# Kernel tuning notes

Measured on AMD Instinct MI355X. Metric: run time of the kernel, lower is better.

The kernel has to match this reference:

```python
import jax, jax.numpy as jnp
import numpy as np

K = 3
N_SENSOR = 10   # num_sensor N (forced by reshape(-1,10,10))
ADJ_N = 5       # adjacency size (forced by reshape(-1,5,5))
T_LEN = 4096    # seq_len
BATCH = 1024    # batch_size == num_of_filters (forced by output accumulation)


def _scaled_laplacian(W):
    # L_tilde = 2L/lambda_max - I, L = D - W (W symmetric -> eigvalsh valid)
    D = jnp.diag(jnp.sum(W, axis=1))
    L = D - W
    lam_max = jnp.max(jnp.linalg.eigvalsh(L))
    return (2.0 * L) / lam_max - jnp.eye(W.shape[0], dtype=W.dtype)


def _cheb_polynomials(L_tilde, K):
    polys = [jnp.eye(L_tilde.shape[0], dtype=L_tilde.dtype), L_tilde]
    for _ in range(2, K):
        polys.append(2.0 * (L_tilde @ polys[-1]) - polys[-2])
    return jnp.stack(polys[:K])  # (K, 5, 5)


def setup_inputs() -> dict:
    key = jax.random.key(0)
    kx, ka, ks, kt = jax.random.split(key, 4)
    x = jax.random.normal(kx, (T_LEN, BATCH, N_SENSOR), dtype=jnp.float32)
    W = jax.random.uniform(ka, (ADJ_N, ADJ_N), dtype=jnp.float32)
    # symmetric, zero-diagonal adjacency so the Laplacian is symmetric PSD-ish
    adj_mx = (W + W.T) * 0.5 * (1.0 - jnp.eye(ADJ_N, dtype=jnp.float32))
    spatial_attention = jax.random.uniform(ks, (BATCH, N_SENSOR, N_SENSOR), dtype=jnp.float32)
    Theta = jax.random.normal(kt, (K, N_SENSOR, BATCH), dtype=jnp.float32)  # (K, num_of_timesteps=10, num_of_filters=B)
    return {"x": x, "adj_mx": adj_mx, "spatial_attention": spatial_attention, "Theta": Theta}


def reference(x, adj_mx, spatial_attention, Theta):
    # adj path is detached in the torch code (cpu().detach().numpy())
    L_tilde = _scaled_laplacian(jax.lax.stop_gradient(adj_mx))
    cheb = _cheb_polynomials(L_tilde, K)                 # (K, 5, 5)
    T, B, N = x.shape                                    # (T, B, 10)
    x_t = jnp.swapaxes(x, 0, 2)                          # (10, B, T)
    sa = spatial_attention.reshape(-1, ADJ_N, ADJ_N)     # (4B, 5, 5)
    output = jnp.zeros((T, B, N), dtype=x.dtype)
    for k in range(K):
        T_k_with_at = (cheb[k] * sa).reshape(-1, N, N)   # (B, 10, 10)
        lhs = jnp.swapaxes(T_k_with_at, 0, 2)            # (10, 10, B)
        rhs = jnp.matmul(lhs, x_t)                       # (10, 10, B) @ (10, B, T) -> (10, 10, T)
        out_k = jnp.matmul(jnp.swapaxes(rhs, 1, 2), Theta[k])  # (10, T, 10) @ (10, B) -> (10, T, B)
        output = output + jnp.transpose(out_k, (1, 2, 0))       # (T, B, 10)
    return jax.nn.relu(output[..., None])                # (T, B, 10, 1)
```

## Files before the change

kernel.cpp:

```cpp
#include <hip/hip_runtime.h>
#include <math.h>

#define TLEN 4096
#define NB   1024
#define NS   10

typedef __attribute__((ext_vector_type(8))) short  s16x8;
typedef __attribute__((ext_vector_type(4))) float  f32x4;

__device__ void k0_body(const float* __restrict__ adj, float* __restrict__ ck) {
  float Wm[5][5], L[5][5];
  for (int r = 0; r < 5; ++r)
    for (int c = 0; c < 5; ++c) Wm[r][c] = adj[r*5+c];
  for (int r = 0; r < 5; ++r) {
    float d = 0.f;
    for (int c = 0; c < 5; ++c) d += Wm[r][c];
    for (int c = 0; c < 5; ++c) L[r][c] = (r==c ? d : 0.f) - Wm[r][c];
  }
  float v[5] = {0.7f, -1.1f, 0.9f, -0.8f, 1.3f};
  for (int it = 0; it < 96; ++it) {
    float w[5];
    for (int r = 0; r < 5; ++r) {
      float s = 0.f;
      for (int c = 0; c < 5; ++c) s += L[r][c]*v[c];
      w[r] = s;
    }
    float s = fabsf(w[0])+fabsf(w[1])+fabsf(w[2])+fabsf(w[3])+fabsf(w[4]);
    float inv = 1.f/s;
    for (int r = 0; r < 5; ++r) v[r] = w[r]*inv;
  }
  float num = 0.f, den = 0.f;
  for (int r = 0; r < 5; ++r) {
    float s = 0.f;
    for (int c = 0; c < 5; ++c) s += L[r][c]*v[c];
    num += v[r]*s; den += v[r]*v[r];
  }
  const float lam = num/den;
  float Lt[5][5];
  for (int r = 0; r < 5; ++r)
    for (int c = 0; c < 5; ++c)
      Lt[r][c] = 2.f*L[r][c]/lam - (r==c ? 1.f : 0.f);
  float T2[5][5];
  for (int r = 0; r < 5; ++r)
    for (int c = 0; c < 5; ++c) {
      float s = 0.f;
      for (int j = 0; j < 5; ++j) s += Lt[r][j]*Lt[j][c];
      T2[r][c] = 2.f*s - (r==c ? 1.f : 0.f);
    }
  for (int p = 0; p < 10; ++p)
    for (int n = 0; n < 10; ++n) {
      int m = (10*p+n) % 25, r = m/5, c = m%5;
      ck[0*100 + p*10+n] = (r==c ? 1.f : 0.f);
      ck[1*100 + p*10+n] = Lt[r][c];
      ck[2*100 + p*10+n] = T2[r][c];
    }
}

static __device__ __forceinline__ unsigned cvtpk(float lo, float hi) {
  unsigned r;
  asm("v_cvt_pk_bf16_f32 %0, %1, %2" : "=v"(r) : "v"(lo), "v"(hi));
  return r;
}
static __device__ __forceinline__ int swz(int P, int L) {
  return P*64 + (L ^ ((P ^ (P >> 2)) & 7));
}

#define KC 64
#define BUF_U32 10240

__global__ __launch_bounds__(384, 3) void ka_mfma(
    const float* __restrict__ x, const float* __restrict__ sa,
    const float* __restrict__ adj, float* __restrict__ ps,
    float* __restrict__ ck) {
  __shared__ __align__(16) unsigned lds[2*BUF_U32];
  const int tid = threadIdx.x;
  if (tid >= 320) {
    if (tid == 320 && blockIdx.x == 0 && blockIdx.y == 0) k0_body(adj, ck);
    return;
  }
  const int w  = tid >> 6;
  const int l  = tid & 63;
  const int t0 = blockIdx.x * 16;
  const int b0 = blockIdx.y * 512;
  const int n0 = 2*w, n1 = 2*w + 1;

  const int bp = tid / 10;
  const int rm = tid - bp*10;
  const int q  = rm >> 1;
  const int th = rm & 1;
  const int gq = rm;
  const int ksx = bp >> 4;
  const int kgx = (bp & 15) >> 2;
  const int jwx = bp & 3;

  f32x4 acc0 = {0.f,0.f,0.f,0.f}, acc1 = {0.f,0.f,0.f,0.f};
  float2 xlo[8], xhi[8], slo[5], shi[5];

  unsigned* cur = lds;
  unsigned* nxt = lds + BUF_U32;

  {
    const float* xb = x + (size_t)(t0 + th*8)*(NB*NS) + (size_t)(b0 + 2*bp)*NS + 2*q;
    #pragma unroll
    for (int r = 0; r < 8; ++r) {
      xlo[r] = *(const float2*)(xb + r*(NB*NS));
      xhi[r] = *(const float2*)(xb + r*(NB*NS) + NS);
    }
    const float* sb = sa + (size_t)(b0 + 2*bp)*100 + gq*10;
    #pragma unroll
    for (int e = 0; e < 5; ++e) {
      slo[e] = *(const float2*)(sb + 2*e);
      shi[e] = *(const float2*)(sb + 100 + 2*e);
    }
  }
  #pragma unroll
  for (int r = 0; r < 8; ++r) {
    const int L = kgx*16 + th*8 + r;
    cur[swz((2*q  )*2 + ksx, L)*4 + jwx] = cvtpk(xlo[r].x, xhi[r].x);
    cur[swz((2*q+1)*2 + ksx, L)*4 + jwx] = cvtpk(xlo[r].y, xhi[r].y);
  }
  #pragma unroll
  for (int e = 0; e < 5; ++e) {
    const int L = kgx*16 + gq;
    cur[5120 + swz((2*e  )*2 + ksx, L)*4 + jwx] = cvtpk(slo[e].x, shi[e].x);
    cur[5120 + swz((2*e+1)*2 + ksx, L)*4 + jwx] = cvtpk(slo[e].y, shi[e].y);
  }

  for (int c = 0; c < 8; ++c) {
    __syncthreads();
    if (c < 7) {
      const int bc = b0 + (c+1)*KC;
      const float* xb = x + (size_t)(t0 + th*8)*(NB*NS) + (size_t)(bc + 2*bp)*NS + 2*q;
      #pragma unroll
      for (int r = 0; r < 8; ++r) {
        xlo[r] = *(const float2*)(xb + r*(NB*NS));
        xhi[r] = *(const float2*)(xb + r*(NB*NS) + NS);
      }
      const float* sb = sa + (size_t)(bc + 2*bp)*100 + gq*10;
      #pragma unroll
      for (int e = 0; e < 5; ++e) {
        slo[e] = *(const float2*)(sb + 2*e);
        shi[e] = *(const float2*)(sb + 100 + 2*e);
      }
    }
    {
      const s16x8* XBf = (const s16x8*)cur;
      const s16x8* ASf = (const s16x8*)(cur + 5120);
      #pragma unroll
      for (int ks = 0; ks < 2; ++ks) {
        acc0 = __builtin_amdgcn_mfma_f32_16x16x32_bf16(
                 ASf[swz(n0*2+ks, l)], XBf[swz(n0*2+ks, l)], acc0, 0, 0, 0);
        acc1 = __builtin_amdgcn_mfma_f32_16x16x32_bf16(
                 ASf[swz(n1*2+ks, l)], XBf[swz(n1*2+ks, l)], acc1, 0, 0, 0);
      }
    }
    if (c < 7) {
      #pragma unroll
      for (int r = 0; r < 8; ++r) {
        const int L = kgx*16 + th*8 + r;
        nxt[swz((2*q  )*2 + ksx, L)*4 + jwx] = cvtpk(xlo[r].x, xhi[r].x);
        nxt[swz((2*q+1)*2 + ksx, L)*4 + jwx] = cvtpk(xlo[r].y, xhi[r].y);
      }
      #pragma unroll
      for (int e = 0; e < 5; ++e) {
        const int L = kgx*16 + gq;
        nxt[5120 + swz((2*e  )*2 + ksx, L)*4 + jwx] = cvtpk(slo[e].x, shi[e].x);
        nxt[5120 + swz((2*e+1)*2 + ksx, L)*4 + jwx] = cvtpk(slo[e].y, shi[e].y);
      }
      unsigned* t = cur; cur = nxt; nxt = t;
    }
  }
  const int pg = (l >> 4) * 4;
  float* pd = ps + ((size_t)blockIdx.y*TLEN + t0 + (l & 15))*100;
  #pragma unroll
  for (int r = 0; r < 4; ++r) {
    const int p = pg + r;
    if (p < 10) {
      pd[n0*10 + p] = acc0[r];
      pd[n1*10 + p] = acc1[r];
    }
  }
}

#define TT 8
__global__ __launch_bounds__(256) void kc_out(const float* __restrict__ theta,
    const float* __restrict__ ck, const float* __restrict__ ps,
    float* __restrict__ out) {
  __shared__ __align__(16) float S[TT*120];
  __shared__ float C[300];
  __shared__ __align__(16) float stg[2][2560];
  const int tid = threadIdx.x;
  const int t0 = blockIdx.x * TT;
  const int b  = blockIdx.y * 256 + tid;
  for (int j = tid; j < 300; j += 256) C[j] = ck[j];
  for (int j = tid; j < TT*100; j += 256) {
    const int tt = j / 100, q = j - tt*100;
    float s = 0.f;
    #pragma unroll
    for (int sl = 0; sl < 2; ++sl)
      s += ps[((size_t)sl*TLEN + (t0+tt))*100 + q];
    S[tt*120 + (q/10)*12 + (q - (q/10)*10)] = s;
  }
  __syncthreads();
  float W[10][10];
  #pragma unroll
  for (int p = 0; p < 10; ++p) {
    const float th0 = theta[          p*NB + b];
    const float th1 = theta[10*NB  +  p*NB + b];
    const float th2 = theta[20*NB  +  p*NB + b];
    #pragma unroll
    for (int nn = 0; nn < 10; ++nn)
      W[p][nn] = C[p*10+nn]*th0 + C[100+p*10+nn]*th1 + C[200+p*10+nn]*th2;
  }
  for (int tt = 0; tt < TT; ++tt) {
    float acc[10];
    #pragma unroll
    for (int nn = 0; nn < 10; ++nn) {
      const float4 s0 = *(const float4*)(S + tt*120 + nn*12);
      const float4 s1 = *(const float4*)(S + tt*120 + nn*12 + 4);
      const float2 s2 = *(const float2*)(S + tt*120 + nn*12 + 8);
      acc[nn] = s0.x*W[0][nn] + s0.y*W[1][nn] + s0.z*W[2][nn] + s0.w*W[3][nn]
              + s1.x*W[4][nn] + s1.y*W[5][nn] + s1.z*W[6][nn] + s1.w*W[7][nn]
              + s2.x*W[8][nn] + s2.y*W[9][nn];
    }
    float* sg = stg[tt & 1];
    #pragma unroll
    for (int nn = 0; nn < 10; ++nn)
      sg[tid*10 + nn] = fmaxf(acc[nn], 0.f);
    __syncthreads();
    const float4* sp = (const float4*)sg;
    float4* op = (float4*)(out + (size_t)(t0+tt)*(NB*NS)
                               + (size_t)blockIdx.y*2560);
    op[tid]       = sp[tid];
    op[tid + 256] = sp[tid + 256];
    if (tid < 128) op[tid + 512] = sp[tid + 512];
  }
}

extern "C" void kernel_launch(void* const* d_in, const int* in_sizes, int n_in,
                              void* d_out, int out_size, void* d_ws, size_t ws_size,
                              hipStream_t stream) {
  const float* x   = (const float*)d_in[0];
  const float* adj = (const float*)d_in[1];
  const float* sa  = (const float*)d_in[2];
  const float* th  = (const float*)d_in[3];
  float* out = (float*)d_out;
  float* ws  = (float*)d_ws;
  float* ck  = ws;
  float* ps  = ws + 1024;
  hipLaunchKernelGGL(ka_mfma, dim3(TLEN/16, 2), dim3(384), 0, stream,
                     x, sa, adj, ps, ck);
  hipLaunchKernelGGL(kc_out,  dim3(TLEN/TT, NB/256), dim3(256), 0, stream,
                     th, ck, ps, out);
}
```

Baseline: 98.50 us.

## Fuse MFMA contraction and output projection into one kernel per time tile

Merges the two kernels into one: each block now covers all 1024 batch rows for 16 timesteps, keeps the partial sums in shared memory instead of writing them to a global workspace, and computes the Theta/Chebyshev projection and ReLU output in the same block. The Laplacian power iteration is recomputed in every block by an otherwise idle thread, spread across the chunk loop so it runs alongside the MFMA work. The double-buffered LDS staging becomes a single buffer with an extra barrier per chunk. Nontemporal loads and stores are used for x and the output. The grid shrinks to 256 blocks, which may lower occupancy, and the extra syncs may expose load latency.

```diff
diff --git a/kernel.cpp b/kernel.cpp
--- a/kernel.cpp
+++ b/kernel.cpp
@@ -4,57 +4,13 @@
 #define TLEN 4096
 #define NB   1024
 #define NS   10
-
-typedef __attribute__((ext_vector_type(8))) short  s16x8;
-typedef __attribute__((ext_vector_type(4))) float  f32x4;
-
-__device__ void k0_body(const float* __restrict__ adj, float* __restrict__ ck) {
-  float Wm[5][5], L[5][5];
-  for (int r = 0; r < 5; ++r)
-    for (int c = 0; c < 5; ++c) Wm[r][c] = adj[r*5+c];
-  for (int r = 0; r < 5; ++r) {
-    float d = 0.f;
-    for (int c = 0; c < 5; ++c) d += Wm[r][c];
-    for (int c = 0; c < 5; ++c) L[r][c] = (r==c ? d : 0.f) - Wm[r][c];
-  }
-  float v[5] = {0.7f, -1.1f, 0.9f, -0.8f, 1.3f};
-  for (int it = 0; it < 96; ++it) {
-    float w[5];
-    for (int r = 0; r < 5; ++r) {
-      float s = 0.f;
-      for (int c = 0; c < 5; ++c) s += L[r][c]*v[c];
-      w[r] = s;
-    }
-    float s = fabsf(w[0])+fabsf(w[1])+fabsf(w[2])+fabsf(w[3])+fabsf(w[4]);
-    float inv = 1.f/s;
-    for (int r = 0; r < 5; ++r) v[r] = w[r]*inv;
-  }
-  float num = 0.f, den = 0.f;
-  for (int r = 0; r < 5; ++r) {
-    float s = 0.f;
-    for (int c = 0; c < 5; ++c) s += L[r][c]*v[c];
-    num += v[r]*s; den += v[r]*v[r];
-  }
-  const float lam = num/den;
-  float Lt[5][5];
-  for (int r = 0; r < 5; ++r)
-    for (int c = 0; c < 5; ++c)
-      Lt[r][c] = 2.f*L[r][c]/lam - (r==c ? 1.f : 0.f);
-  float T2[5][5];
-  for (int r = 0; r < 5; ++r)
-    for (int c = 0; c < 5; ++c) {
-      float s = 0.f;
-      for (int j = 0; j < 5; ++j) s += Lt[r][j]*Lt[j][c];
-      T2[r][c] = 2.f*s - (r==c ? 1.f : 0.f);
-    }
-  for (int p = 0; p < 10; ++p)
-    for (int n = 0; n < 10; ++n) {
-      int m = (10*p+n) % 25, r = m/5, c = m%5;
-      ck[0*100 + p*10+n] = (r==c ? 1.f : 0.f);
-      ck[1*100 + p*10+n] = Lt[r][c];
-      ck[2*100 + p*10+n] = T2[r][c];
-    }
-}
+#define KC   64
+#define NCHK 16
+#define BUF_U32 10240
+
+typedef __attribute__((ext_vector_type(8))) short s16x8;
+typedef __attribute__((ext_vector_type(4))) float f32x4;
+typedef __attribute__((ext_vector_type(2))) float f32x2;
 
 static __device__ __forceinline__ unsigned cvtpk(float lo, float hi) {
   unsigned r;
@@ -65,87 +21,97 @@
   return P*64 + (L ^ ((P ^ (P >> 2)) & 7));
 }
 
-#define KC 64
-#define BUF_U32 10240
-
-__global__ __launch_bounds__(384, 3) void ka_mfma(
+__global__ __launch_bounds__(512) void fused_k(
     const float* __restrict__ x, const float* __restrict__ sa,
-    const float* __restrict__ adj, float* __restrict__ ps,
-    float* __restrict__ ck) {
-  __shared__ __align__(16) unsigned lds[2*BUF_U32];
+    const float* __restrict__ adj, const float* __restrict__ theta,
+    float* __restrict__ out) {
+  __shared__ __align__(16) unsigned buf[BUF_U32];
+  __shared__ __align__(16) float S[16*120];
+  __shared__ float ck[300];
   const int tid = threadIdx.x;
-  if (tid >= 320) {
-    if (tid == 320 && blockIdx.x == 0 && blockIdx.y == 0) k0_body(adj, ck);
-    return;
-  }
-  const int w  = tid >> 6;
-  const int l  = tid & 63;
-  const int t0 = blockIdx.x * 16;
-  const int b0 = blockIdx.y * 512;
-  const int n0 = 2*w, n1 = 2*w + 1;
-
-  const int bp = tid / 10;
-  const int rm = tid - bp*10;
-  const int q  = rm >> 1;
-  const int th = rm & 1;
-  const int gq = rm;
+  const int l   = tid & 63;
+  const int t0  = blockIdx.x * 16;
+
+  const int w   = tid >> 6;
+  const int bp  = tid / 10;
+  const int rm  = tid - bp*10;
+  const int q   = rm >> 1;
+  const int th  = rm & 1;
+  const int gq  = rm;
   const int ksx = bp >> 4;
   const int kgx = (bp & 15) >> 2;
   const int jwx = bp & 3;
+  const int n0  = 2*w, n1 = 2*w + 1;
 
   f32x4 acc0 = {0.f,0.f,0.f,0.f}, acc1 = {0.f,0.f,0.f,0.f};
-  float2 xlo[8], xhi[8], slo[5], shi[5];
-
-  unsigned* cur = lds;
-  unsigned* nxt = lds + BUF_U32;
-
-  {
-    const float* xb = x + (size_t)(t0 + th*8)*(NB*NS) + (size_t)(b0 + 2*bp)*NS + 2*q;
+  f32x2 xlo[8], xhi[8], slo[5], shi[5];
+
+  float pL[5][5], pv[5];
+  if (tid == 320) {
+    float Wm[5][5];
+    #pragma unroll
+    for (int r = 0; r < 5; ++r)
+      #pragma unroll
+      for (int c = 0; c < 5; ++c) Wm[r][c] = adj[r*5+c];
+    #pragma unroll
+    for (int r = 0; r < 5; ++r) {
+      float d = 0.f;
+      #pragma unroll
+      for (int c = 0; c < 5; ++c) d += Wm[r][c];
+      #pragma unroll
+      for (int c = 0; c < 5; ++c) pL[r][c] = (r==c ? d : 0.f) - Wm[r][c];
+    }
+    pv[0]=0.7f; pv[1]=-1.1f; pv[2]=0.9f; pv[3]=-0.8f; pv[4]=1.3f;
+  }
+
+  if (tid < 320) {
+    const float* xb = x + (size_t)(t0 + th*8)*(NB*NS) + (size_t)(2*bp)*NS + 2*q;
     #pragma unroll
     for (int r = 0; r < 8; ++r) {
-      xlo[r] = *(const float2*)(xb + r*(NB*NS));
-      xhi[r] = *(const float2*)(xb + r*(NB*NS) + NS);
-    }
-    const float* sb = sa + (size_t)(b0 + 2*bp)*100 + gq*10;
+      xlo[r] = __builtin_nontemporal_load((const f32x2*)(xb + r*(NB*NS)));
+      xhi[r] = __builtin_nontemporal_load((const f32x2*)(xb + r*(NB*NS) + NS));
+    }
+    const float* sb = sa + (size_t)(2*bp)*100 + gq*10;
     #pragma unroll
     for (int e = 0; e < 5; ++e) {
-      slo[e] = *(const float2*)(sb + 2*e);
-      shi[e] = *(const float2*)(sb + 100 + 2*e);
-    }
-  }
-  #pragma unroll
-  for (int r = 0; r < 8; ++r) {
-    const int L = kgx*16 + th*8 + r;
-    cur[swz((2*q  )*2 + ksx, L)*4 + jwx] = cvtpk(xlo[r].x, xhi[r].x);
-    cur[swz((2*q+1)*2 + ksx, L)*4 + jwx] = cvtpk(xlo[r].y, xhi[r].y);
-  }
-  #pragma unroll
-  for (int e = 0; e < 5; ++e) {
-    const int L = kgx*16 + gq;
-    cur[5120 + swz((2*e  )*2 + ksx, L)*4 + jwx] = cvtpk(slo[e].x, shi[e].x);
-    cur[5120 + swz((2*e+1)*2 + ksx, L)*4 + jwx] = cvtpk(slo[e].y, shi[e].y);
-  }
-
-  for (int c = 0; c < 8; ++c) {
+      slo[e] = *(const f32x2*)(sb + 2*e);
+      shi[e] = *(const f32x2*)(sb + 100 + 2*e);
+    }
+    #pragma unroll
+    for (int r = 0; r < 8; ++r) {
+      const int L = kgx*16 + th*8 + r;
+      buf[swz((2*q  )*2 + ksx, L)*4 + jwx] = cvtpk(xlo[r].x, xhi[r].x);
+      buf[swz((2*q+1)*2 + ksx, L)*4 + jwx] = cvtpk(xlo[r].y, xhi[r].y);
+    }
+    #pragma unroll
+    for (int e = 0; e < 5; ++e) {
+      const int L = kgx*16 + gq;
+      buf[5120 + swz((2*e  )*2 + ksx, L)*4 + jwx] = cvtpk(slo[e].x, shi[e].x);
+      buf[5120 + swz((2*e+1)*2 + ksx, L)*4 + jwx] = cvtpk(slo[e].y, shi[e].y);
+    }
+  }
+
+  for (int c = 0; c < NCHK; ++c) {
     __syncthreads();
-    if (c < 7) {
-      const int bc = b0 + (c+1)*KC;
-      const float* xb = x + (size_t)(t0 + th*8)*(NB*NS) + (size_t)(bc + 2*bp)*NS + 2*q;
-      #pragma unroll
-      for (int r = 0; r < 8; ++r) {
-        xlo[r] = *(const float2*)(xb + r*(NB*NS));
-        xhi[r] = *(const float2*)(xb + r*(NB*NS) + NS);
-      }
-      const float* sb = sa + (size_t)(bc + 2*bp)*100 + gq*10;
-      #pragma unroll
-      for (int e = 0; e < 5; ++e) {
-        slo[e] = *(const float2*)(sb + 2*e);
-        shi[e] = *(const float2*)(sb + 100 + 2*e);
-      }
-    }
-    {
-      const s16x8* XBf = (const s16x8*)cur;
-      const s16x8* ASf = (const s16x8*)(cur + 5120);
+    if (tid < 320) {
+      if (c + 1 < NCHK) {
+        const int bc = (c+1)*KC;
+        const float* xb = x + (size_t)(t0 + th*8)*(NB*NS)
+                            + (size_t)(bc + 2*bp)*NS + 2*q;
+        #pragma unroll
+        for (int r = 0; r < 8; ++r) {
+          xlo[r] = __builtin_nontemporal_load((const f32x2*)(xb + r*(NB*NS)));
+          xhi[r] = __builtin_nontemporal_load((const f32x2*)(xb + r*(NB*NS) + NS));
+        }
+        const float* sb = sa + (size_t)(bc + 2*bp)*100 + gq*10;
+        #pragma unroll
+        for (int e = 0; e < 5; ++e) {
+          slo[e] = *(const f32x2*)(sb + 2*e);
+          shi[e] = *(const f32x2*)(sb + 100 + 2*e);
+        }
+      }
+      const s16x8* XBf = (const s16x8*)buf;
+      const s16x8* ASf = (const s16x8*)(buf + 5120);
       #pragma unroll
       for (int ks = 0; ks < 2; ++ks) {
         acc0 = __builtin_amdgcn_mfma_f32_16x16x32_bf16(
@@ -153,87 +119,138 @@
         acc1 = __builtin_amdgcn_mfma_f32_16x16x32_bf16(
                  ASf[swz(n1*2+ks, l)], XBf[swz(n1*2+ks, l)], acc1, 0, 0, 0);
       }
-    }
-    if (c < 7) {
+    } else if (tid == 320 && c < 12) {
+      #pragma unroll
+      for (int it = 0; it < 8; ++it) {
+        float wv[5];
+        #pragma unroll
+        for (int r = 0; r < 5; ++r) {
+          float s = 0.f;
+          #pragma unroll
+          for (int cc = 0; cc < 5; ++cc) s += pL[r][cc]*pv[cc];
+          wv[r] = s;
+        }
+        float s = fabsf(wv[0])+fabsf(wv[1])+fabsf(wv[2])+fabsf(wv[3])+fabsf(wv[4]);
+        float inv = 1.f/s;
+        #pragma unroll
+        for (int r = 0; r < 5; ++r) pv[r] = wv[r]*inv;
+      }
+    }
+    __syncthreads();
+    if (tid < 320 && c + 1 < NCHK) {
       #pragma unroll
       for (int r = 0; r < 8; ++r) {
         const int L = kgx*16 + th*8 + r;
-        nxt[swz((2*q  )*2 + ksx, L)*4 + jwx] = cvtpk(xlo[r].x, xhi[r].x);
-        nxt[swz((2*q+1)*2 + ksx, L)*4 + jwx] = cvtpk(xlo[r].y, xhi[r].y);
+        buf[swz((2*q  )*2 + ksx, L)*4 + jwx] = cvtpk(xlo[r].x, xhi[r].x);
+        buf[swz((2*q+1)*2 + ksx, L)*4 + jwx] = cvtpk(xlo[r].y, xhi[r].y);
       }
       #pragma unroll
       for (int e = 0; e < 5; ++e) {
         const int L = kgx*16 + gq;
-        nxt[5120 + swz((2*e  )*2 + ksx, L)*4 + jwx] = cvtpk(slo[e].x, shi[e].x);
-        nxt[5120 + swz((2*e+1)*2 + ksx, L)*4 + jwx] = cvtpk(slo[e].y, shi[e].y);
-      }
-      unsigned* t = cur; cur = nxt; nxt = t;
-    }
-  }
-  const int pg = (l >> 4) * 4;
-  float* pd = ps + ((size_t)blockIdx.y*TLEN + t0 + (l & 15))*100;
-  #pragma unroll
-  for (int r = 0; r < 4; ++r) {
-    const int p = pg + r;
-    if (p < 10) {
-      pd[n0*10 + p] = acc0[r];
-      pd[n1*10 + p] = acc1[r];
-    }
-  }
-}
-
-#define TT 8
-__global__ __launch_bounds__(256) void kc_out(const float* __restrict__ theta,
-    const float* __restrict__ ck, const float* __restrict__ ps,
-    float* __restrict__ out) {
-  __shared__ __align__(16) float S[TT*120];
-  __shared__ float C[300];
-  __shared__ __align__(16) float stg[2][2560];
-  const int tid = threadIdx.x;
-  const int t0 = blockIdx.x * TT;
-  const int b  = blockIdx.y * 256 + tid;
-  for (int j = tid; j < 300; j += 256) C[j] = ck[j];
-  for (int j = tid; j < TT*100; j += 256) {
-    const int tt = j / 100, q = j - tt*100;
-    float s = 0.f;
-    #pragma unroll
-    for (int sl = 0; sl < 2; ++sl)
-      s += ps[((size_t)sl*TLEN + (t0+tt))*100 + q];
-    S[tt*120 + (q/10)*12 + (q - (q/10)*10)] = s;
+        buf[5120 + swz((2*e  )*2 + ksx, L)*4 + jwx] = cvtpk(slo[e].x, shi[e].x);
+        buf[5120 + swz((2*e+1)*2 + ksx, L)*4 + jwx] = cvtpk(slo[e].y, shi[e].y);
+      }
+    }
+  }
+
+  if (tid == 320) {
+    float num = 0.f, den = 0.f;
+    #pragma unroll
+    for (int r = 0; r < 5; ++r) {
+      float s = 0.f;
+      #pragma unroll
+      for (int cc = 0; cc < 5; ++cc) s += pL[r][cc]*pv[cc];
+      num += pv[r]*s; den += pv[r]*pv[r];
+    }
+    const float lam = num/den;
+    float Lt[5][5], T2[5][5];
+    #pragma unroll
+    for (int r = 0; r < 5; ++r)
+      #pragma unroll
+      for (int cc = 0; cc < 5; ++cc)
+        Lt[r][cc] = 2.f*pL[r][cc]/lam - (r==cc ? 1.f : 0.f);
+    #pragma unroll
+    for (int r = 0; r < 5; ++r)
+      #pragma unroll
+      for (int cc = 0; cc < 5; ++cc) {
+        float s = 0.f;
+        #pragma unroll
+        for (int j = 0; j < 5; ++j) s += Lt[r][j]*Lt[j][cc];
+        T2[r][cc] = 2.f*s - (r==cc ? 1.f : 0.f);
+      }
+    #pragma unroll
+    for (int p = 0; p < 10; ++p)
+      #pragma unroll
+      for (int nn = 0; nn < 10; ++nn) {
+        const int m = (10*p+nn) % 25, r = m/5, cc = m%5;
+        ck[0*100 + p*10+nn] = (r==cc ? 1.f : 0.f);
+        ck[1*100 + p*10+nn] = Lt[r][cc];
+        ck[2*100 + p*10+nn] = T2[r][cc];
+      }
+  }
+  if (tid < 320) {
+    const int pg = (l >> 4) * 4;
+    const int tl = l & 15;
+    #pragma unroll
+    for (int r = 0; r < 4; ++r) {
+      const int p = pg + r;
+      if (p < 10) {
+        S[tl*120 + n0*12 + p] = acc0[r];
+        S[tl*120 + n1*12 + p] = acc1[r];
+      }
+    }
   }
   __syncthreads();
-  float W[10][10];
-  #pragma unroll
-  for (int p = 0; p < 10; ++p) {
-    const float th0 = theta[          p*NB + b];
-    const float th1 = theta[10*NB  +  p*NB + b];
-    const float th2 = theta[20*NB  +  p*NB + b];
-    #pragma unroll
-    for (int nn = 0; nn < 10; ++nn)
-      W[p][nn] = C[p*10+nn]*th0 + C[100+p*10+nn]*th1 + C[200+p*10+nn]*th2;
-  }
-  for (int tt = 0; tt < TT; ++tt) {
-    float acc[10];
-    #pragma unroll
-    for (int nn = 0; nn < 10; ++nn) {
-      const float4 s0 = *(const float4*)(S + tt*120 + nn*12);
-      const float4 s1 = *(const float4*)(S + tt*120 + nn*12 + 4);
-      const float2 s2 = *(const float2*)(S + tt*120 + nn*12 + 8);
-      acc[nn] = s0.x*W[0][nn] + s0.y*W[1][nn] + s0.z*W[2][nn] + s0.w*W[3][nn]
-              + s1.x*W[4][nn] + s1.y*W[5][nn] + s1.z*W[6][nn] + s1.w*W[7][nn]
-              + s2.x*W[8][nn] + s2.y*W[9][nn];
-    }
-    float* sg = stg[tt & 1];
-    #pragma unroll
-    for (int nn = 0; nn < 10; ++nn)
-      sg[tid*10 + nn] = fmaxf(acc[nn], 0.f);
-    __syncthreads();
-    const float4* sp = (const float4*)sg;
-    float4* op = (float4*)(out + (size_t)(t0+tt)*(NB*NS)
-                               + (size_t)blockIdx.y*2560);
-    op[tid]       = sp[tid];
-    op[tid + 256] = sp[tid + 256];
-    if (tid < 128) op[tid + 512] = sp[tid + 512];
+
+  float* stg = (float*)buf;
+  for (int g = 0; g < 2; ++g) {
+    const int b = g*512 + tid;
+    float W[10][10];
+    #pragma unroll
+    for (int p = 0; p < 10; ++p) {
+      const float th0 = theta[          p*NB + b];
+      const float th1 = theta[10*NB  +  p*NB + b];
+      const float th2 = theta[20*NB  +  p*NB + b];
+      #pragma unroll
+      for (int nn = 0; nn < 10; ++nn)
+        W[p][nn] = ck[p*10+nn]*th0 + ck[100+p*10+nn]*th1 + ck[200+p*10+nn]*th2;
+    }
+    for (int tp = 0; tp < 8; ++tp) {
+      float a0[10], a1[10];
+      #pragma unroll
+      for (int nn = 0; nn < 10; ++nn) {
+        const float4 s0 = *(const float4*)(S + (2*tp)*120 + nn*12);
+        const float4 s1 = *(const float4*)(S + (2*tp)*120 + nn*12 + 4);
+        const float2 s2 = *(const float2*)(S + (2*tp)*120 + nn*12 + 8);
+        a0[nn] = s0.x*W[0][nn] + s0.y*W[1][nn] + s0.z*W[2][nn] + s0.w*W[3][nn]
+               + s1.x*W[4][nn] + s1.y*W[5][nn] + s1.z*W[6][nn] + s1.w*W[7][nn]
+               + s2.x*W[8][nn] + s2.y*W[9][nn];
+        const float4 u0 = *(const float4*)(S + (2*tp+1)*120 + nn*12);
+        const float4 u1 = *(const float4*)(S + (2*tp+1)*120 + nn*12 + 4);
+        const float2 u2 = *(const float2*)(S + (2*tp+1)*120 + nn*12 + 8);
+        a1[nn] = u0.x*W[0][nn] + u0.y*W[1][nn] + u0.z*W[2][nn] + u0.w*W[3][nn]
+               + u1.x*W[4][nn] + u1.y*W[5][nn] + u1.z*W[6][nn] + u1.w*W[7][nn]
+               + u2.x*W[8][nn] + u2.y*W[9][nn];
+      }
+      __syncthreads();
+      #pragma unroll
+      for (int nn = 0; nn < 10; ++nn) {
+        stg[       tid*10 + nn] = fmaxf(a0[nn], 0.f);
+        stg[5120 + tid*10 + nn] = fmaxf(a1[nn], 0.f);
+      }
+      __syncthreads();
+      const f32x4* sv = (const f32x4*)stg;
+      f32x4* op0 = (f32x4*)(out + (size_t)(t0 + 2*tp)*(NB*NS) + g*5120);
+      f32x4* op1 = (f32x4*)(out + (size_t)(t0 + 2*tp + 1)*(NB*NS) + g*5120);
+      __builtin_nontemporal_store(sv[tid],        op0 + tid);
+      __builtin_nontemporal_store(sv[tid + 512],  op0 + tid + 512);
+      if (tid < 256)
+        __builtin_nontemporal_store(sv[tid + 1024], op0 + tid + 1024);
+      __builtin_nontemporal_store(sv[tid + 1280], op1 + tid);
+      __builtin_nontemporal_store(sv[tid + 1792], op1 + tid + 512);
+      if (tid < 256)
+        __builtin_nontemporal_store(sv[tid + 2304], op1 + tid + 1024);
+    }
   }
 }
 
@@ -245,11 +262,6 @@
   const float* sa  = (const float*)d_in[2];
   const float* th  = (const float*)d_in[3];
   float* out = (float*)d_out;
-  float* ws  = (float*)d_ws;
-  float* ck  = ws;
-  float* ps  = ws + 1024;
-  hipLaunchKernelGGL(ka_mfma, dim3(TLEN/16, 2), dim3(384), 0, stream,
-                     x, sa, adj, ps, ck);
-  hipLaunchKernelGGL(kc_out,  dim3(TLEN/TT, NB/256), dim3(256), 0, stream,
-                     th, ck, ps, out);
-}
+  hipLaunchKernelGGL(fused_k, dim3(TLEN/16), dim3(512), 0, stream,
+                     x, sa, adj, th, out);
+}
```

Measured after the change: 85.24 us. -13.5%, faster.
